# Kernel optimization log

Hardware: AMD Instinct MI355X
Metric: run time of the kernel (lower is better)

The kernel has to match this reference:

```python
import jax, jax.numpy as jnp
import numpy as np
import math

LATENT_D = 64
NDIM = 2
VEC = LATENT_D // 4          # 16 output rows per hyper-generated weight
D_LAT = 64                   # channels-proj input dim (latent last dim)
POSENC_CH = 31               # nerf posenc: 1 + 2*15 per coordinate
CH = [NDIM * POSENC_CH, VEC, VEC, VEC]  # [62, 16, 16, 16]
N_PTS = 32768
BATCH = 16
LN_EPS = 1e-5


def posenc_nerf(x, min_deg=0, max_deg=15):
    # x: [..., D] -> [..., D*(1 + 2*(max_deg-min_deg))]
    scales = 2.0 ** jnp.arange(min_deg, max_deg, dtype=x.dtype)
    xb = (x[..., None, :] * scales[:, None]).reshape(*x.shape[:-1], -1)
    emb = jnp.sin(jnp.concatenate([xb, xb + jnp.pi / 2.0], axis=-1))
    return jnp.concatenate([x, emb], axis=-1)


def layernorm(h, w, b):
    mu = h.mean(-1, keepdims=True)
    var = ((h - mu) ** 2).mean(-1, keepdims=True)
    return (h - mu) / jnp.sqrt(var + LN_EPS) * w + b


def setup_inputs() -> dict:
    key = jax.random.key(0)
    ks = iter(jax.random.split(key, 40))
    inp = {}
    inp["x"] = jax.random.uniform(next(ks), (N_PTS, NDIM), dtype=jnp.float32)
    inp["latent"] = jax.random.normal(next(ks), (BATCH, LATENT_D, D_LAT), dtype=jnp.float32)
    for i, ch in enumerate(CH):
        s = 1.0 / math.sqrt(D_LAT)
        inp[f"pw{i}"] = jax.random.normal(next(ks), (VEC * ch, D_LAT), dtype=jnp.float32) * s
        inp[f"pb{i}"] = jax.random.normal(next(ks), (VEC * ch,), dtype=jnp.float32) * 0.01
        inp[f"lnw{i}"] = jnp.full((ch,), 0.0625, dtype=jnp.float32)  # learned_scale init
        inp[f"lnb{i}"] = jnp.zeros((ch,), dtype=jnp.float32)
        inp[f"mb{i}"] = jax.random.normal(next(ks), (VEC,), dtype=jnp.float32)  # registered bias (randn init)
    dims = [(100, VEC), (100, 100), (1, 100)]
    for j, (o, i_) in enumerate(dims, 1):
        s = 1.0 / math.sqrt(i_)
        inp[f"w{j}"] = jax.random.uniform(next(ks), (o, i_), dtype=jnp.float32, minval=-s, maxval=s)
        inp[f"b{j}"] = jax.random.uniform(next(ks), (o,), dtype=jnp.float32, minval=-s, maxval=s)
    return inp


def reference(x, latent,
              pw0, pb0, lnw0, lnb0, mb0,
              pw1, pb1, lnw1, lnb1, mb1,
              pw2, pb2, lnw2, lnb2, mb2,
              pw3, pb3, lnw3, lnb3, mb3,
              w1, b1, w2, b2, w3, b3):
    B = latent.shape[0]
    # x[None].repeat(B,1,1) then nerf-encode: [B, N, 62]
    h = posenc_nerf(jnp.broadcast_to(x[None], (B,) + x.shape))
    proj = [(pw0, pb0, lnw0, lnb0, mb0), (pw1, pb1, lnw1, lnb1, mb1),
            (pw2, pb2, lnw2, lnb2, mb2), (pw3, pb3, lnw3, lnb3, mb3)]
    start = 0
    for (pw, pb, lnw, lnb, mb), ch in zip(proj, CH):
        lat = latent[:, start:start + VEC, :]           # [B, 16, 64]
        start += VEC
        # ChannelsProj: einsum + LN(channels) + bias -> per-sample weight [B, 16, ch]
        wv = jnp.einsum('bvd,vcd->bvc', lat, pw.reshape(VEC, ch, D_LAT))
        wv = layernorm(wv, lnw, lnb) + pb.reshape(VEC, ch)
        # hyper-MLP stage: bmm + bias + SiLU
        h = jax.nn.silu(jnp.einsum('bpi,boi->bpo', h, wv) + mb)
    # trailing dense MLP: 16 -> 100 -> 100 -> 1
    h = jax.nn.silu(h @ w1.T + b1)
    h = jax.nn.silu(h @ w2.T + b2)
    h = h @ w3.T + b3
    return h.squeeze(-1)  # [B, N]
```

## Files before the change

kernel.cpp:

```cpp
#include <hip/hip_runtime.h>

#define N_PTS 32768
#define BATCH 16
#define PIO2F 1.5707963705062866f

typedef __attribute__((ext_vector_type(8))) _Float16 half8;
typedef __attribute__((ext_vector_type(4))) _Float16 half4;
typedef __attribute__((ext_vector_type(4))) float f32x4;

__device__ __forceinline__ float silu_f(float v) {
    return v * __builtin_amdgcn_rcpf(1.0f + __expf(-v));
}

__device__ __forceinline__ float wave_sum(float v) {
    #pragma unroll
    for (int off = 1; off < 64; off <<= 1) v += __shfl_xor(v, off, 64);
    return v;
}

__device__ __forceinline__ void lds_fence() {
    asm volatile("" ::: "memory");
#if __has_builtin(__builtin_amdgcn_wave_barrier)
    __builtin_amdgcn_wave_barrier();
#else
    __builtin_amdgcn_sched_barrier(0);
#endif
    asm volatile("" ::: "memory");
}

__device__ __forceinline__ f32x4 mfma16h(half8 a, half8 b, f32x4 c) {
    return __builtin_amdgcn_mfma_f32_16x16x32_f16(a, b, c, 0, 0, 0);
}

__device__ __forceinline__ half8 h8zero() {
    half8 z;
    #pragma unroll
    for (int r = 0; r < 8; ++r) z[r] = (_Float16)0.0f;
    return z;
}

__global__ void wv_kernel(
    const float* __restrict__ latent,
    const float* __restrict__ pw0, const float* __restrict__ pb0,
    const float* __restrict__ lnw0, const float* __restrict__ lnb0,
    const float* __restrict__ pw1, const float* __restrict__ pb1,
    const float* __restrict__ lnw1, const float* __restrict__ lnb1,
    const float* __restrict__ pw2, const float* __restrict__ pb2,
    const float* __restrict__ lnw2, const float* __restrict__ lnb2,
    const float* __restrict__ pw3, const float* __restrict__ pb3,
    const float* __restrict__ lnw3, const float* __restrict__ lnb3,
    float* __restrict__ wvb) {
    int blk = blockIdx.x;
    int l = blk >> 8;
    int rest = blk & 255;
    int b = rest >> 4, o = rest & 15;
    int c = threadIdx.x;

    const float *pw, *pb, *lnw, *lnb;
    float* outp;
    int ch;
    switch (l) {
        case 0:  pw = pw0; pb = pb0; lnw = lnw0; lnb = lnb0; outp = wvb;                 ch = 62; break;
        case 1:  pw = pw1; pb = pb1; lnw = lnw1; lnb = lnb1; outp = wvb + 15872;         ch = 16; break;
        case 2:  pw = pw2; pb = pb2; lnw = lnw2; lnb = lnb2; outp = wvb + 15872 + 4096;  ch = 16; break;
        default: pw = pw3; pb = pb3; lnw = lnw3; lnb = lnb3; outp = wvb + 15872 + 8192;  ch = 16; break;
    }
    const float* lat = latent + ((size_t)(b * 64 + l * 16 + o)) * 64;
    float dot = 0.f;
    if (c < ch) {
        const float* pr = pw + ((size_t)(o * ch + c)) * 64;
        #pragma unroll
        for (int d0 = 0; d0 < 64; d0++) dot += lat[d0] * pr[d0];
    }
    float act = (c < ch) ? dot : 0.f;
    float mu = wave_sum(act) * (1.0f / ch);
    float diff = (c < ch) ? (dot - mu) : 0.f;
    float var = wave_sum(diff * diff) * (1.0f / ch);
    float norm = diff * rsqrtf(var + 1e-5f);
    if (c < ch) outp[(size_t)(b * 16 + o) * ch + c] = norm * lnw[c] + lnb[c] + pb[o * ch + c];
}

__global__ __launch_bounds__(256) void posenc_pre(
    const float* __restrict__ xg, _Float16* __restrict__ peh) {
    int p = blockIdx.x * 256 + threadIdx.x;
    float x0 = xg[2 * p], x1 = xg[2 * p + 1];
    size_t pbs = (size_t)(p >> 4) * 1024 + (size_t)(p & 15) * 8;
    #pragma unroll
    for (int c = 0; c < 8; ++c) {
        half8 hv;
        #pragma unroll
        for (int j = 0; j < 8; ++j) {
            float v;
            if (c < 4) {
                int f = 8 * c + j;
                int idx2 = f - 2;
                int s = idx2 >> 1;
                float sc = __uint_as_float((unsigned)(127 + s) << 23);
                float xa = (idx2 & 1) ? x1 : x0;
                v = sinf(xa * sc);
                if (f == 0) v = x0;
                if (f == 1) v = x1;
            } else {
                int t = 8 * (c - 4) + j;
                int s = t >> 1;
                float sc = __uint_as_float((unsigned)(127 + s) << 23);
                float xa = (t & 1) ? x1 : x0;
                v = sinf(fmaf(xa, sc, PIO2F));
                if (t >= 30) v = 0.f;
            }
            hv[j] = (_Float16)v;
        }
        *(half8*)(peh + pbs + c * 128) = hv;
    }
}

#define BOUNCE_OFF  0
#define W2H_OFF     20480
#define W1H_OFF     41280
#define WV0H_OFF    46656
#define WVH_OFF     48960
#define B1_OFF      51264
#define B2_OFF      51712
#define W3_OFF      52160
#define MB_LDS_OFF  52608
#define LDS_TOTAL   52864

template <bool PRE>
__global__ __launch_bounds__(512, 2) void mfma_kernel(
    const float* __restrict__ xg,
    const _Float16* __restrict__ peh,
    const float* __restrict__ wvb,
    const float* __restrict__ mb0, const float* __restrict__ mb1,
    const float* __restrict__ mb2, const float* __restrict__ mb3,
    const float* __restrict__ w1, const float* __restrict__ b1,
    const float* __restrict__ w2, const float* __restrict__ b2,
    const float* __restrict__ w3, const float* __restrict__ b3,
    float* __restrict__ out) {
    extern __shared__ char smem[];
    _Float16* lds_bounce = (_Float16*)(smem + BOUNCE_OFF);
    _Float16* lds_w2h    = (_Float16*)(smem + W2H_OFF);
    _Float16* lds_w1h    = (_Float16*)(smem + W1H_OFF);
    _Float16* lds_wv0h   = (_Float16*)(smem + WV0H_OFF);
    _Float16* lds_wvh    = (_Float16*)(smem + WVH_OFF);
    float*    lds_b1     = (float*)(smem + B1_OFF);
    float*    lds_b2     = (float*)(smem + B2_OFF);
    float*    lds_w3     = (float*)(smem + W3_OFF);
    float*    lds_mb     = (float*)(smem + MB_LDS_OFF);

    const int b  = blockIdx.x >> 6;
    const int p0 = (blockIdx.x & 63) * 512;

    for (int idx = threadIdx.x; idx < 100 * 104; idx += 512) {
        int o = idx / 104, k = idx - o * 104;
        lds_w2h[idx] = (_Float16)((k < 100) ? w2[o * 100 + k] : 0.f);
    }
    for (int idx = threadIdx.x; idx < 112 * 24; idx += 512) {
        int o = idx / 24, k = idx - o * 24;
        lds_w1h[idx] = (_Float16)((o < 100 && k < 16) ? w1[o * 16 + k] : 0.f);
    }
    const float* wv0g = wvb + b * 992;
    for (int idx = threadIdx.x; idx < 16 * 72; idx += 512) {
        int o = idx / 72, k = idx - o * 72;
        lds_wv0h[idx] = (_Float16)((k < 62) ? wv0g[o * 62 + k] : 0.f);
    }
    const float* wv1g = wvb + 15872 + b * 256;
    const float* wv2g = wvb + 15872 + 4096 + b * 256;
    const float* wv3g = wvb + 15872 + 8192 + b * 256;
    for (int idx = threadIdx.x; idx < 3 * 16 * 24; idx += 512) {
        int li = idx / 384, rest = idx - li * 384;
        int o = rest / 24, k = rest - o * 24;
        const float* src = (li == 0) ? wv1g : (li == 1) ? wv2g : wv3g;
        lds_wvh[idx] = (_Float16)((k < 16) ? src[o * 16 + k] : 0.f);
    }
    if (threadIdx.x < 112) {
        int o = threadIdx.x;
        lds_b1[o] = (o < 100) ? b1[o] : 0.f;
        lds_b2[o] = (o < 100) ? b2[o] : 0.f;
        lds_w3[o] = (o < 100) ? w3[o] : 0.f;
    }
    if (threadIdx.x >= 128 && threadIdx.x < 192) {
        int t = threadIdx.x - 128;
        int li = t >> 4, o = t & 15;
        const float* mbp = (li == 0) ? mb0 : (li == 1) ? mb1 : (li == 2) ? mb2 : mb3;
        lds_mb[t] = mbp[o];
    }
    __syncthreads();

    const int l    = threadIdx.x & 63;
    const int w    = threadIdx.x >> 6;
    const int lrow = l & 15;
    const int lkg  = l >> 4;
    _Float16* bwA = lds_bounce + w * 1280;
    _Float16* bwB = bwA + 640;
    const int pbase = w * 64;
    const float b3v = b3[0];
    const int ptg0 = (p0 + pbase) >> 4;
    const bool kmask = (lkg >= 2);

    #pragma unroll 1
    for (int it = 0; it < 2; ++it) {
        const int ptA = it * 2, ptB = ptA + 1;
        const int pcolA = p0 + pbase + ptA * 16 + lrow;
        const int pcolB = pcolA + 16;

        half8 pb0A, pb1A, pb0B, pb1B;
        if (PRE) {
            size_t baseA = (size_t)(ptg0 + ptA) * 1024 + (size_t)lkg * 128 + (size_t)lrow * 8;
            pb0A = *(const half8*)(peh + baseA);
            pb1A = *(const half8*)(peh + baseA + 512);
            pb0B = *(const half8*)(peh + baseA + 1024);
            pb1B = *(const half8*)(peh + baseA + 1536);
        } else {
            #pragma unroll
            for (int ch = 0; ch < 2; ++ch) {
                const int pc = ch ? pcolB : pcolA;
                const float x0 = xg[2 * pc], x1 = xg[2 * pc + 1];
                half8 t0, t1;
                #pragma unroll
                for (int j = 0; j < 8; ++j) {
                    int idx2 = 8 * lkg + j - 2;
                    int s = idx2 >> 1;
                    float sc = __uint_as_float((unsigned)(127 + s) << 23);
                    float xa = (idx2 & 1) ? x1 : x0;
                    float v = sinf(xa * sc);
                    if (lkg == 0 && j == 0) v = x0;
                    if (lkg == 0 && j == 1) v = x1;
                    t0[j] = (_Float16)v;
                }
                #pragma unroll
                for (int j = 0; j < 8; ++j) {
                    int t = 8 * lkg + j;
                    int s = t >> 1;
                    float sc = __uint_as_float((unsigned)(127 + s) << 23);
                    float xa = (t & 1) ? x1 : x0;
                    float v = sinf(fmaf(xa, sc, PIO2F));
                    if (t >= 30) v = 0.f;
                    t1[j] = (_Float16)v;
                }
                if (ch) { pb0B = t0; pb1B = t1; } else { pb0A = t0; pb1A = t1; }
            }
        }

        f32x4 accA = *(const f32x4*)(lds_mb + lkg * 4);
        f32x4 accB = accA;
        {
            half8 a0 = *(const half8*)(lds_wv0h + lrow * 72 + lkg * 8);
            accA = mfma16h(a0, pb0A, accA);
            accB = mfma16h(a0, pb0B, accB);
            a0 = *(const half8*)(lds_wv0h + lrow * 72 + 32 + lkg * 8);
            accA = mfma16h(a0, pb1A, accA);
            accB = mfma16h(a0, pb1B, accB);
        }

        #pragma unroll
        for (int li = 0; li < 3; ++li) {
            half4 hvA, hvB;
            #pragma unroll
            for (int r = 0; r < 4; ++r) {
                hvA[r] = (_Float16)silu_f(accA[r]);
                hvB[r] = (_Float16)silu_f(accB[r]);
            }
            lds_fence();
            *(half4*)(bwA + lrow * 40 + lkg * 4) = hvA;
            *(half4*)(bwB + lrow * 40 + lkg * 4) = hvB;
            lds_fence();
            half8 fA = *(const half8*)(bwA + lrow * 40 + (lkg & 1) * 8);
            half8 fB = *(const half8*)(bwB + lrow * 40 + (lkg & 1) * 8);
            f32x4 bias = *(const f32x4*)(lds_mb + (li + 1) * 16 + lkg * 4);
            half8 ah = *(const half8*)(lds_wvh + (li * 16 + lrow) * 24 + (lkg & 1) * 8);
            if (kmask) ah = h8zero();
            accA = mfma16h(ah, fA, bias);
            accB = mfma16h(ah, fB, bias);
        }
        {
            half4 hvA, hvB;
            #pragma unroll
            for (int r = 0; r < 4; ++r) {
                hvA[r] = (_Float16)silu_f(accA[r]);
                hvB[r] = (_Float16)silu_f(accB[r]);
            }
            lds_fence();
            *(half4*)(bwA + lrow * 40 + lkg * 4) = hvA;
            *(half4*)(bwB + lrow * 40 + lkg * 4) = hvB;
            lds_fence();
        }
        half8 hbfA = *(const half8*)(bwA + lrow * 40 + (lkg & 1) * 8);
        half8 hbfB = *(const half8*)(bwB + lrow * 40 + (lkg & 1) * 8);

        f32x4 a2A[7], a2B[7];
        #pragma unroll
        for (int f2 = 0; f2 < 7; ++f2) {
            f32x4 bias = *(const f32x4*)(lds_b2 + f2 * 16 + lkg * 4);
            a2A[f2] = bias;
            a2B[f2] = bias;
        }
        #pragma unroll
        for (int ks = 0; ks < 4; ++ks) {
            lds_fence();
            #pragma unroll
            for (int lf = 0; lf < 2; ++lf) {
                const int fmt = 2 * ks + lf;
                if (fmt < 7) {
                    f32x4 bias = *(const f32x4*)(lds_b1 + fmt * 16 + lkg * 4);
                    half8 ah = *(const half8*)(lds_w1h + (fmt * 16 + lrow) * 24 + (lkg & 1) * 8);
                    if (kmask) ah = h8zero();
                    f32x4 a1A = mfma16h(ah, hbfA, bias);
                    f32x4 a1B = mfma16h(ah, hbfB, bias);
                    half4 hvA, hvB;
                    #pragma unroll
                    for (int r = 0; r < 4; ++r) {
                        hvA[r] = (_Float16)silu_f(a1A[r]);
                        hvB[r] = (_Float16)silu_f(a1B[r]);
                    }
                    *(half4*)(bwA + lrow * 40 + lf * 16 + lkg * 4) = hvA;
                    *(half4*)(bwB + lrow * 40 + lf * 16 + lkg * 4) = hvB;
                } else {
                    half4 hz;
                    #pragma unroll
                    for (int r = 0; r < 4; ++r) hz[r] = (_Float16)0.0f;
                    *(half4*)(bwA + lrow * 40 + lf * 16 + lkg * 4) = hz;
                    *(half4*)(bwB + lrow * 40 + lf * 16 + lkg * 4) = hz;
                }
            }
            lds_fence();
            half8 h2fA = *(const half8*)(bwA + lrow * 40 + lkg * 8);
            half8 h2fB = *(const half8*)(bwB + lrow * 40 + lkg * 8);
            const int kb = ks * 32 + lkg * 8;
            const int kba = (ks == 3) ? ((kb > 96) ? 96 : kb) : kb;
            #pragma unroll
            for (int f2 = 0; f2 < 7; ++f2) {
                int arow = f2 * 16 + lrow;
                if (f2 == 6) arow = (arow > 99) ? 99 : arow;
                half8 ah = *(const half8*)(lds_w2h + arow * 104 + kba);
                a2A[f2] = mfma16h(ah, h2fA, a2A[f2]);
                a2B[f2] = mfma16h(ah, h2fB, a2B[f2]);
            }
        }

        float outA = 0.f, outB = 0.f;
        #pragma unroll
        for (int f2 = 0; f2 < 7; ++f2) {
            f32x4 w3v = *(const f32x4*)(lds_w3 + f2 * 16 + lkg * 4);
            #pragma unroll
            for (int r = 0; r < 4; ++r) {
                outA = fmaf(silu_f(a2A[f2][r]), w3v[r], outA);
                outB = fmaf(silu_f(a2B[f2][r]), w3v[r], outB);
            }
        }
        outA += __shfl_xor(outA, 16, 64);
        outA += __shfl_xor(outA, 32, 64);
        outB += __shfl_xor(outB, 16, 64);
        outB += __shfl_xor(outB, 32, 64);
        if (l < 16) {
            out[(size_t)b * N_PTS + pcolA] = outA + b3v;
            out[(size_t)b * N_PTS + pcolB] = outB + b3v;
        }
    }
}

extern "C" void kernel_launch(void* const* d_in, const int* in_sizes, int n_in,
                              void* d_out, int out_size, void* d_ws, size_t ws_size,
                              hipStream_t stream) {
    const float* x = (const float*)d_in[0];
    const float* latent = (const float*)d_in[1];
    const float *pw[4], *pb[4], *lnw[4], *lnb[4], *mb[4];
    for (int l = 0; l < 4; l++) {
        pw[l]  = (const float*)d_in[2 + 5 * l];
        pb[l]  = (const float*)d_in[3 + 5 * l];
        lnw[l] = (const float*)d_in[4 + 5 * l];
        lnb[l] = (const float*)d_in[5 + 5 * l];
        mb[l]  = (const float*)d_in[6 + 5 * l];
    }
    const float* w1 = (const float*)d_in[22];
    const float* b1 = (const float*)d_in[23];
    const float* w2 = (const float*)d_in[24];
    const float* b2 = (const float*)d_in[25];
    const float* w3 = (const float*)d_in[26];
    const float* b3 = (const float*)d_in[27];

    float* wvb = (float*)d_ws;
    _Float16* peh = (_Float16*)((char*)d_ws + 112640);
    const size_t WS_NEED = 112640 + (size_t)N_PTS * 64 * sizeof(_Float16);
    bool pre = ws_size >= WS_NEED;

    wv_kernel<<<1024, 64, 0, stream>>>(latent,
        pw[0], pb[0], lnw[0], lnb[0],
        pw[1], pb[1], lnw[1], lnb[1],
        pw[2], pb[2], lnw[2], lnb[2],
        pw[3], pb[3], lnw[3], lnb[3],
        wvb);

    if (pre) {
        posenc_pre<<<N_PTS / 256, 256, 0, stream>>>(x, peh);
        hipFuncSetAttribute((const void*)mfma_kernel<true>,
                            hipFuncAttributeMaxDynamicSharedMemorySize, LDS_TOTAL);
        mfma_kernel<true><<<BATCH * (N_PTS / 512), 512, LDS_TOTAL, stream>>>(
            x, peh, wvb, mb[0], mb[1], mb[2], mb[3],
            w1, b1, w2, b2, w3, b3, (float*)d_out);
    } else {
        hipFuncSetAttribute((const void*)mfma_kernel<false>,
                            hipFuncAttributeMaxDynamicSharedMemorySize, LDS_TOTAL);
        mfma_kernel<false><<<BATCH * (N_PTS / 512), 512, LDS_TOTAL, stream>>>(
            x, peh, wvb, mb[0], mb[1], mb[2], mb[3],
            w1, b1, w2, b2, w3, b3, (float*)d_out);
    }
}
```

Before: 74.82 us.

## Hoist all posenc loads upfront, raise occupancy bound, prioritize MFMA loop

Moves the per-tile MLP body into a lambda, and in the precomputed-encoding path issues all eight global half8 loads before either compute pass so the second pair's memory latency hides behind the first pass. It also raises the launch-bounds occupancy hint from 2 to 6 blocks per CU, which caps registers per thread, and wraps the W2 MFMA block in s_setprio to favour matrix issue. The tighter register budget risks spills given the 28 accumulator vectors, and LDS use (about 52 KB per block) may limit how many blocks actually fit per CU.

```diff
diff --git a/kernel.cpp b/kernel.cpp
--- a/kernel.cpp
+++ b/kernel.cpp
@@ -126,7 +126,7 @@
 #define LDS_TOTAL   52864
 
 template <bool PRE>
-__global__ __launch_bounds__(512, 2) void mfma_kernel(
+__global__ __launch_bounds__(512, 6) void mfma_kernel(
     const float* __restrict__ xg,
     const _Float16* __restrict__ peh,
     const float* __restrict__ wvb,
@@ -197,23 +197,146 @@
     const int ptg0 = (p0 + pbase) >> 4;
     const bool kmask = (lkg >= 2);
 
-    #pragma unroll 1
-    for (int it = 0; it < 2; ++it) {
-        const int ptA = it * 2, ptB = ptA + 1;
-        const int pcolA = p0 + pbase + ptA * 16 + lrow;
-        const int pcolB = pcolA + 16;
-
-        half8 pb0A, pb1A, pb0B, pb1B;
-        if (PRE) {
-            size_t baseA = (size_t)(ptg0 + ptA) * 1024 + (size_t)lkg * 128 + (size_t)lrow * 8;
-            pb0A = *(const half8*)(peh + baseA);
-            pb1A = *(const half8*)(peh + baseA + 512);
-            pb0B = *(const half8*)(peh + baseA + 1024);
-            pb1B = *(const half8*)(peh + baseA + 1536);
-        } else {
+    auto pipe = [&](half8 pb0A, half8 pb1A, half8 pb0B, half8 pb1B,
+                    int pcolA, int pcolB) {
+        f32x4 accA = *(const f32x4*)(lds_mb + lkg * 4);
+        f32x4 accB = accA;
+        {
+            half8 a0 = *(const half8*)(lds_wv0h + lrow * 72 + lkg * 8);
+            accA = mfma16h(a0, pb0A, accA);
+            accB = mfma16h(a0, pb0B, accB);
+            a0 = *(const half8*)(lds_wv0h + lrow * 72 + 32 + lkg * 8);
+            accA = mfma16h(a0, pb1A, accA);
+            accB = mfma16h(a0, pb1B, accB);
+        }
+
+        #pragma unroll
+        for (int li = 0; li < 3; ++li) {
+            half4 hvA, hvB;
+            #pragma unroll
+            for (int r = 0; r < 4; ++r) {
+                hvA[r] = (_Float16)silu_f(accA[r]);
+                hvB[r] = (_Float16)silu_f(accB[r]);
+            }
+            lds_fence();
+            *(half4*)(bwA + lrow * 40 + lkg * 4) = hvA;
+            *(half4*)(bwB + lrow * 40 + lkg * 4) = hvB;
+            lds_fence();
+            half8 fA = *(const half8*)(bwA + lrow * 40 + (lkg & 1) * 8);
+            half8 fB = *(const half8*)(bwB + lrow * 40 + (lkg & 1) * 8);
+            f32x4 bias = *(const f32x4*)(lds_mb + (li + 1) * 16 + lkg * 4);
+            half8 ah = *(const half8*)(lds_wvh + (li * 16 + lrow) * 24 + (lkg & 1) * 8);
+            if (kmask) ah = h8zero();
+            accA = mfma16h(ah, fA, bias);
+            accB = mfma16h(ah, fB, bias);
+        }
+        {
+            half4 hvA, hvB;
+            #pragma unroll
+            for (int r = 0; r < 4; ++r) {
+                hvA[r] = (_Float16)silu_f(accA[r]);
+                hvB[r] = (_Float16)silu_f(accB[r]);
+            }
+            lds_fence();
+            *(half4*)(bwA + lrow * 40 + lkg * 4) = hvA;
+            *(half4*)(bwB + lrow * 40 + lkg * 4) = hvB;
+            lds_fence();
+        }
+        half8 hbfA = *(const half8*)(bwA + lrow * 40 + (lkg & 1) * 8);
+        half8 hbfB = *(const half8*)(bwB + lrow * 40 + (lkg & 1) * 8);
+
+        f32x4 a2A[7], a2B[7];
+        #pragma unroll
+        for (int f2 = 0; f2 < 7; ++f2) {
+            f32x4 bias = *(const f32x4*)(lds_b2 + f2 * 16 + lkg * 4);
+            a2A[f2] = bias;
+            a2B[f2] = bias;
+        }
+        #pragma unroll
+        for (int ks = 0; ks < 4; ++ks) {
+            lds_fence();
+            #pragma unroll
+            for (int lf = 0; lf < 2; ++lf) {
+                const int fmt = 2 * ks + lf;
+                if (fmt < 7) {
+                    f32x4 bias = *(const f32x4*)(lds_b1 + fmt * 16 + lkg * 4);
+                    half8 ah = *(const half8*)(lds_w1h + (fmt * 16 + lrow) * 24 + (lkg & 1) * 8);
+                    if (kmask) ah = h8zero();
+                    f32x4 a1A = mfma16h(ah, hbfA, bias);
+                    f32x4 a1B = mfma16h(ah, hbfB, bias);
+                    half4 hvA, hvB;
+                    #pragma unroll
+                    for (int r = 0; r < 4; ++r) {
+                        hvA[r] = (_Float16)silu_f(a1A[r]);
+                        hvB[r] = (_Float16)silu_f(a1B[r]);
+                    }
+                    *(half4*)(bwA + lrow * 40 + lf * 16 + lkg * 4) = hvA;
+                    *(half4*)(bwB + lrow * 40 + lf * 16 + lkg * 4) = hvB;
+                } else {
+                    half4 hz;
+                    #pragma unroll
+                    for (int r = 0; r < 4; ++r) hz[r] = (_Float16)0.0f;
+                    *(half4*)(bwA + lrow * 40 + lf * 16 + lkg * 4) = hz;
+                    *(half4*)(bwB + lrow * 40 + lf * 16 + lkg * 4) = hz;
+                }
+            }
+            lds_fence();
+            half8 h2fA = *(const half8*)(bwA + lrow * 40 + lkg * 8);
+            half8 h2fB = *(const half8*)(bwB + lrow * 40 + lkg * 8);
+            const int kb = ks * 32 + lkg * 8;
+            const int kba = (ks == 3) ? ((kb > 96) ? 96 : kb) : kb;
+            __builtin_amdgcn_s_setprio(1);
+            #pragma unroll
+            for (int f2 = 0; f2 < 7; ++f2) {
+                int arow = f2 * 16 + lrow;
+                if (f2 == 6) arow = (arow > 99) ? 99 : arow;
+                half8 ah = *(const half8*)(lds_w2h + arow * 104 + kba);
+                a2A[f2] = mfma16h(ah, h2fA, a2A[f2]);
+                a2B[f2] = mfma16h(ah, h2fB, a2B[f2]);
+            }
+            __builtin_amdgcn_s_setprio(0);
+        }
+
+        float outA = 0.f, outB = 0.f;
+        #pragma unroll
+        for (int f2 = 0; f2 < 7; ++f2) {
+            f32x4 w3v = *(const f32x4*)(lds_w3 + f2 * 16 + lkg * 4);
+            #pragma unroll
+            for (int r = 0; r < 4; ++r) {
+                outA = fmaf(silu_f(a2A[f2][r]), w3v[r], outA);
+                outB = fmaf(silu_f(a2B[f2][r]), w3v[r], outB);
+            }
+        }
+        outA += __shfl_xor(outA, 16, 64);
+        outA += __shfl_xor(outA, 32, 64);
+        outB += __shfl_xor(outB, 16, 64);
+        outB += __shfl_xor(outB, 32, 64);
+        if (l < 16) {
+            out[(size_t)b * N_PTS + pcolA] = outA + b3v;
+            out[(size_t)b * N_PTS + pcolB] = outB + b3v;
+        }
+    };
+
+    const int pA0 = p0 + pbase + lrow;
+    if (PRE) {
+        size_t base0 = (size_t)ptg0 * 1024 + (size_t)lkg * 128 + (size_t)lrow * 8;
+        half8 f00 = *(const half8*)(peh + base0);
+        half8 f01 = *(const half8*)(peh + base0 + 512);
+        half8 f10 = *(const half8*)(peh + base0 + 1024);
+        half8 f11 = *(const half8*)(peh + base0 + 1536);
+        half8 f20 = *(const half8*)(peh + base0 + 2048);
+        half8 f21 = *(const half8*)(peh + base0 + 2560);
+        half8 f30 = *(const half8*)(peh + base0 + 3072);
+        half8 f31 = *(const half8*)(peh + base0 + 3584);
+        pipe(f00, f01, f10, f11, pA0, pA0 + 16);
+        pipe(f20, f21, f30, f31, pA0 + 32, pA0 + 48);
+    } else {
+        #pragma unroll 1
+        for (int it = 0; it < 2; ++it) {
+            half8 fr[4];
             #pragma unroll
             for (int ch = 0; ch < 2; ++ch) {
-                const int pc = ch ? pcolB : pcolA;
+                const int pc = pA0 + it * 32 + ch * 16;
                 const float x0 = xg[2 * pc], x1 = xg[2 * pc + 1];
                 half8 t0, t1;
                 #pragma unroll
@@ -237,123 +360,10 @@
                     if (t >= 30) v = 0.f;
                     t1[j] = (_Float16)v;
                 }
-                if (ch) { pb0B = t0; pb1B = t1; } else { pb0A = t0; pb1A = t1; }
-            }
-        }
-
-        f32x4 accA = *(const f32x4*)(lds_mb + lkg * 4);
-        f32x4 accB = accA;
-        {
-            half8 a0 = *(const half8*)(lds_wv0h + lrow * 72 + lkg * 8);
-            accA = mfma16h(a0, pb0A, accA);
-            accB = mfma16h(a0, pb0B, accB);
-            a0 = *(const half8*)(lds_wv0h + lrow * 72 + 32 + lkg * 8);
-            accA = mfma16h(a0, pb1A, accA);
-            accB = mfma16h(a0, pb1B, accB);
-        }
-
-        #pragma unroll
-        for (int li = 0; li < 3; ++li) {
-            half4 hvA, hvB;
-            #pragma unroll
-            for (int r = 0; r < 4; ++r) {
-                hvA[r] = (_Float16)silu_f(accA[r]);
-                hvB[r] = (_Float16)silu_f(accB[r]);
-            }
-            lds_fence();
-            *(half4*)(bwA + lrow * 40 + lkg * 4) = hvA;
-            *(half4*)(bwB + lrow * 40 + lkg * 4) = hvB;
-            lds_fence();
-            half8 fA = *(const half8*)(bwA + lrow * 40 + (lkg & 1) * 8);
-            half8 fB = *(const half8*)(bwB + lrow * 40 + (lkg & 1) * 8);
-            f32x4 bias = *(const f32x4*)(lds_mb + (li + 1) * 16 + lkg * 4);
-            half8 ah = *(const half8*)(lds_wvh + (li * 16 + lrow) * 24 + (lkg & 1) * 8);
-            if (kmask) ah = h8zero();
-            accA = mfma16h(ah, fA, bias);
-            accB = mfma16h(ah, fB, bias);
-        }
-        {
-            half4 hvA, hvB;
-            #pragma unroll
-            for (int r = 0; r < 4; ++r) {
-                hvA[r] = (_Float16)silu_f(accA[r]);
-                hvB[r] = (_Float16)silu_f(accB[r]);
-            }
-            lds_fence();
-            *(half4*)(bwA + lrow * 40 + lkg * 4) = hvA;
-            *(half4*)(bwB + lrow * 40 + lkg * 4) = hvB;
-            lds_fence();
-        }
-        half8 hbfA = *(const half8*)(bwA + lrow * 40 + (lkg & 1) * 8);
-        half8 hbfB = *(const half8*)(bwB + lrow * 40 + (lkg & 1) * 8);
-
-        f32x4 a2A[7], a2B[7];
-        #pragma unroll
-        for (int f2 = 0; f2 < 7; ++f2) {
-            f32x4 bias = *(const f32x4*)(lds_b2 + f2 * 16 + lkg * 4);
-            a2A[f2] = bias;
-            a2B[f2] = bias;
-        }
-        #pragma unroll
-        for (int ks = 0; ks < 4; ++ks) {
-            lds_fence();
-            #pragma unroll
-            for (int lf = 0; lf < 2; ++lf) {
-                const int fmt = 2 * ks + lf;
-                if (fmt < 7) {
-                    f32x4 bias = *(const f32x4*)(lds_b1 + fmt * 16 + lkg * 4);
-                    half8 ah = *(const half8*)(lds_w1h + (fmt * 16 + lrow) * 24 + (lkg & 1) * 8);
-                    if (kmask) ah = h8zero();
-                    f32x4 a1A = mfma16h(ah, hbfA, bias);
-                    f32x4 a1B = mfma16h(ah, hbfB, bias);
-                    half4 hvA, hvB;
-                    #pragma unroll
-                    for (int r = 0; r < 4; ++r) {
-                        hvA[r] = (_Float16)silu_f(a1A[r]);
-                        hvB[r] = (_Float16)silu_f(a1B[r]);
-                    }
-                    *(half4*)(bwA + lrow * 40 + lf * 16 + lkg * 4) = hvA;
-                    *(half4*)(bwB + lrow * 40 + lf * 16 + lkg * 4) = hvB;
-                } else {
-                    half4 hz;
-                    #pragma unroll
-                    for (int r = 0; r < 4; ++r) hz[r] = (_Float16)0.0f;
-                    *(half4*)(bwA + lrow * 40 + lf * 16 + lkg * 4) = hz;
-                    *(half4*)(bwB + lrow * 40 + lf * 16 + lkg * 4) = hz;
-                }
-            }
-            lds_fence();
-            half8 h2fA = *(const half8*)(bwA + lrow * 40 + lkg * 8);
-            half8 h2fB = *(const half8*)(bwB + lrow * 40 + lkg * 8);
-            const int kb = ks * 32 + lkg * 8;
-            const int kba = (ks == 3) ? ((kb > 96) ? 96 : kb) : kb;
-            #pragma unroll
-            for (int f2 = 0; f2 < 7; ++f2) {
-                int arow = f2 * 16 + lrow;
-                if (f2 == 6) arow = (arow > 99) ? 99 : arow;
-                half8 ah = *(const half8*)(lds_w2h + arow * 104 + kba);
-                a2A[f2] = mfma16h(ah, h2fA, a2A[f2]);
-                a2B[f2] = mfma16h(ah, h2fB, a2B[f2]);
-            }
-        }
-
-        float outA = 0.f, outB = 0.f;
-        #pragma unroll
-        for (int f2 = 0; f2 < 7; ++f2) {
-            f32x4 w3v = *(const f32x4*)(lds_w3 + f2 * 16 + lkg * 4);
-            #pragma unroll
-            for (int r = 0; r < 4; ++r) {
-                outA = fmaf(silu_f(a2A[f2][r]), w3v[r], outA);
-                outB = fmaf(silu_f(a2B[f2][r]), w3v[r], outB);
-            }
-        }
-        outA += __shfl_xor(outA, 16, 64);
-        outA += __shfl_xor(outA, 32, 64);
-        outB += __shfl_xor(outB, 16, 64);
-        outB += __shfl_xor(outB, 32, 64);
-        if (l < 16) {
-            out[(size_t)b * N_PTS + pcolA] = outA + b3v;
-            out[(size_t)b * N_PTS + pcolB] = outB + b3v;
+                fr[ch * 2] = t0;
+                fr[ch * 2 + 1] = t1;
+            }
+            pipe(fr[0], fr[1], fr[2], fr[3], pA0 + it * 32, pA0 + it * 32 + 16);
         }
     }
 }
```

Result: slower. 98.38 us (+31.5%).
